# Performance work log

Hardware: AMD Instinct MI355X
Metric: run time of the kernel (lower is better)

The kernel has to match this reference:

```python
import jax, jax.numpy as jnp
import numpy as np
from jax.ops import segment_sum, segment_max

LRELU = 0.01  # torch F.leaky_relu default negative_slope


def _seg_softmax(e, seg, n):
    # torch_geometric.utils.softmax: stable segment softmax with 1e-16 eps
    m = segment_max(e, seg, num_segments=n)
    ex = jnp.exp(e - m[seg])
    s = segment_sum(ex, seg, num_segments=n)
    return ex / (s[seg] + 1e-16)


def _gcn(x, ei, w):
    j, i = ei[0], ei[1]  # code unpacks (edge_index_j, edge_index_i)
    n = x.shape[0]
    deg = segment_sum(jnp.ones_like(x[:, 0])[i], i, num_segments=n)
    dis = jnp.where(deg > 0, deg ** -0.5, 0.0)
    norm = dis[j] * dis[i]
    agg = segment_sum(norm[:, None] * x[j], i, num_segments=n)  # out[i] += norm*x[j]
    return jax.nn.relu(agg) @ w


def _highway(x1, x2, w, b):
    gate = jax.nn.sigmoid(x1 @ w + b)
    return gate * x2 + (1.0 - gate) * x1


def _gat_r(x, ei, a_i, a_j):
    j, i = ei[0], ei[1]
    n = x.shape[0]
    si = x @ a_i  # [R]
    sj = x @ a_j
    e = si[i] + sj[j]
    alpha = _seg_softmax(jax.nn.leaky_relu(e, LRELU).astype(jnp.float32), j, n)  # grouped by j!
    return jax.nn.relu(segment_sum(alpha[:, None] * x[j], i, num_segments=n))


def _graphattention_wjq(x, ei, rel_all, rel_emb, ww1):
    i, j = ei[0], ei[1]  # this module unpacks (i, j)
    n = x.shape[0]
    ef = jax.nn.leaky_relu(x, LRELU)
    re = jax.nn.leaky_relu(rel_emb, LRELU)
    feat = jnp.concatenate([ef[i], re[rel_all], ef[j]], axis=1)  # [E, 700]
    att = _seg_softmax(feat @ ww1, i, n)
    return segment_sum(feat * att[:, None], i, num_segments=n)  # [N, 700]


def _gat(x, r, ei, rel, a_i, a_j, a_r):
    j, i = ei[0], ei[1]
    n = x.shape[0]
    e = (x @ a_i)[i] + (x @ a_j)[j] + (r @ a_r)[rel]
    alpha = _seg_softmax(jax.nn.leaky_relu(e, LRELU).astype(jnp.float32), i, n)
    return jax.nn.relu(segment_sum(alpha[:, None] * x[j], i, num_segments=n))


def setup_inputs() -> dict:
    key = jax.random.key(0)
    ks = jax.random.split(key, 24)
    N, E, R, ELG, EH, RH = 20000, 150000, 1000, 15000, 300, 100

    def edges(k, n_nodes, n_edges):
        k1, k2 = jax.random.split(k)
        src = jax.random.randint(k1, (n_edges,), 0, n_nodes)
        dst = jax.random.randint(k2, (n_edges,), 0, n_nodes)
        src = jnp.where(src == dst, (src + 1) % n_nodes, src)  # no self-loops
        ring = jnp.arange(n_nodes)  # guarantee in-degree >= 1 everywhere
        src = src.at[:n_nodes].set((ring + 1) % n_nodes)
        dst = dst.at[:n_nodes].set(ring)
        return jnp.stack([src, dst])  # row0 = j (source), row1 = i (target)

    rel = jax.random.randint(ks[3], (E,), 0, R).at[0].set(R - 1)  # branch -> rel_emb1
    p = lambda k, sh: (jax.random.normal(k, sh, jnp.float32) * 0.05)
    return {
        "x_e": jax.random.normal(ks[0], (N, EH), jnp.float32),
        "edge_index": edges(ks[1], N, E),
        "rel": rel,
        "edge_index_all": edges(ks[2], N, E),
        "rel_all": jax.random.randint(ks[4], (E,), 0, 2 * R),
        "line_graph_index_out": edges(ks[5], R, ELG),
        "line_graph_val_out": jax.random.normal(ks[6], (ELG,), jnp.float32),
        "line_graph_index_in": edges(ks[7], R, ELG),
        "line_graph_val_in": jax.random.normal(ks[8], (ELG,), jnp.float32),
        "gcn1_w": p(ks[9], (EH, EH)),
        "gcn2_w": p(ks[10], (EH, EH)),
        "hw1_w": p(ks[11], (EH, EH)),
        "hw1_b": jnp.zeros((EH,), jnp.float32),
        "hw2_w": p(ks[12], (EH, EH)),
        "hw2_b": jnp.zeros((EH,), jnp.float32),
        "ww1": p(ks[13], (2 * EH + RH,)),
        "gat_ai": p(ks[14], (2 * (2 * EH + RH) - 400 + 0,)) if False else p(ks[14], (1000,)),
        "gat_aj": p(ks[15], (1000,)),
        "gat_ar": p(ks[16], (RH,)),
        "gatr_ai": p(ks[17], (RH,)),
        "gatr_aj": p(ks[18], (RH,)),
        "rel_emb1": p(ks[19], (R, RH)),
        "rel_emb2": p(ks[20], (R, RH)),
    }


def reference(x_e, edge_index, rel, edge_index_all, rel_all,
              line_graph_index_out, line_graph_val_out,
              line_graph_index_in, line_graph_val_in,
              gcn1_w, gcn2_w, hw1_w, hw1_b, hw2_w, hw2_b, ww1,
              gat_ai, gat_aj, gat_ar, gatr_ai, gatr_aj, rel_emb1, rel_emb2):
    # RAGA.forward; inputs constructed so rel.max()+1 == rel_emb1.shape[0]
    # (branch taken) and edge_index_all has no self-loops (remove_self_loops no-op).
    x = _highway(x_e, _gcn(x_e, edge_index_all, gcn1_w), hw1_w, hw1_b)
    x = _highway(x, _gcn(x, edge_index_all, gcn2_w), hw2_w, hw2_b)
    rel_emb_out = _gat_r(rel_emb1, line_graph_index_out, gatr_ai, gatr_aj)
    rel_emb_in = _gat_r(rel_emb1, line_graph_index_in, gatr_ai, gatr_aj)
    rel_emb = jnp.concatenate([rel_emb_out, rel_emb_in], axis=0)  # [2R, 100]
    x_wjq = jnp.concatenate(
        [x, _graphattention_wjq(x, edge_index_all, rel_all, rel_emb, ww1)], axis=1)  # [N, 1000]
    out = jnp.concatenate(
        [x_wjq, _gat(x_wjq, rel_emb, edge_index_all, rel_all, gat_ai, gat_aj, gat_ar)], axis=1)
    return out  # [N, 2000]
```

## Files before the change

kernel.cpp:

```cpp
#include <hip/hip_runtime.h>
#include <math.h>

#define LSL 0.01f

typedef _Float16 half8 __attribute__((ext_vector_type(8)));
typedef _Float16 half2 __attribute__((ext_vector_type(2)));
typedef float floatx4 __attribute__((ext_vector_type(4)));

static __device__ __forceinline__ float lrelu_f(float x){ return x > 0.f ? x : LSL * x; }
static __device__ __forceinline__ void atomAddF(float* p, float v){ unsafeAtomicAdd(p, v); }

static __device__ __forceinline__ unsigned encF(float f){
  unsigned u = __float_as_uint(f);
  return (u & 0x80000000u) ? ~u : (u | 0x80000000u);
}
static __device__ __forceinline__ float decF(unsigned u){
  return (u & 0x80000000u) ? __uint_as_float(u & 0x7FFFFFFFu) : __uint_as_float(~u);
}

__global__ void k_count2(const int* __restrict__ dstA, const int* __restrict__ srcA,
                         int* __restrict__ degD, int* __restrict__ degS, int E){
  int e = blockIdx.x * blockDim.x + threadIdx.x;
  if (e < E){ atomicAdd(degD + dstA[e], 1); atomicAdd(degS + srcA[e], 1); }
}

__global__ __launch_bounds__(1024)
void k_scan2(const int* __restrict__ cntD, int* __restrict__ offD,
             const int* __restrict__ cntS, int* __restrict__ offS, int n){
  const int* cnt = blockIdx.x ? cntS : cntD;
  int* off = blockIdx.x ? offS : offD;
  int t = threadIdx.x, lane = t & 63, wid = t >> 6;
  int len = (n + 1023) >> 10;
  int lo = t * len, hi = min(lo + len, n);
  int s = 0;
  for (int k = lo; k < hi; k++) s += cnt[k];
  int ws = s;
  #pragma unroll
  for (int o = 1; o < 64; o <<= 1){
    int u = __shfl_up(ws, o);
    if (lane >= o) ws += u;
  }
  __shared__ int wtot[16];
  if (lane == 63) wtot[wid] = ws;
  __syncthreads();
  int wpre = 0;
  #pragma unroll
  for (int k2 = 0; k2 < 16; k2++) wpre += (k2 < wid) ? wtot[k2] : 0;
  int run = wpre + ws - s;
  for (int k = lo; k < hi; k++){ off[k] = run; run += cnt[k]; }
  if (t == 0){
    int tot = 0;
    #pragma unroll
    for (int k2 = 0; k2 < 16; k2++) tot += wtot[k2];
    off[n] = tot;
  }
}

__global__ void k_fill2(const int* __restrict__ dstA, const int* __restrict__ srcA,
                        const int* __restrict__ offD, const int* __restrict__ offS,
                        int* __restrict__ curD, int* __restrict__ curS,
                        int* __restrict__ permD, int* __restrict__ permS, int E){
  int e = blockIdx.x * blockDim.x + threadIdx.x;
  if (e >= E) return;
  int i = dstA[e];
  permD[offD[i] + atomicAdd(curD + i, 1)] = e;
  int j = srcA[e];
  permS[offS[j] + atomicAdd(curS + j, 1)] = e;
}

__global__ void k_inv_sqrt_int(const int* __restrict__ deg, float* __restrict__ dis, int N){
  int v = blockIdx.x * blockDim.x + threadIdx.x;
  if (v < N){ int d = deg[v]; dis[v] = d > 0 ? rsqrtf((float)d) : 0.f; }
}

__global__ __launch_bounds__(256)
void k_conv_f16(const float* __restrict__ x, _Float16* __restrict__ xh, int N){
  int i = blockIdx.x, t = threadIdx.x;
  _Float16* o = xh + (size_t)i * 320;
  if (i < N){
    const float* r = x + (size_t)i * 300;
    o[t] = (_Float16)r[t];
    if (t < 44) o[t + 256] = (_Float16)r[t + 256];
    else if (t < 64) o[t + 256] = (_Float16)0.f;
  } else {
    o[t] = (_Float16)0.f;
    if (t < 64) o[t + 256] = (_Float16)0.f;
  }
}

__global__ __launch_bounds__(256)
void k_gcn_gather(const int* __restrict__ off, const int* __restrict__ perm,
                  const int* __restrict__ src, const _Float16* __restrict__ x,
                  const float* __restrict__ dis, _Float16* __restrict__ agg, int N){
  int i = (int)(((long)blockIdx.x * blockDim.x + threadIdx.x) >> 6);
  int lane = threadIdx.x & 63;
  if (i >= N) return;
  int p0 = off[i], p1 = off[i+1];
  float di = dis[i];
  float acc[8] = {0.f,0.f,0.f,0.f,0.f,0.f,0.f,0.f};
  for (int base = p0; base < p1; base += 64){
    int m = min(64, p1 - base);
    int jj = 0; float wl = 0.f;
    if (base + lane < p1){
      int e = perm[base + lane];
      jj = src[e];
      wl = di * dis[jj];
    }
    int q = 0;
    for (; q + 1 < m; q += 2){
      int j0 = __shfl(jj, q),   j1 = __shfl(jj, q+1);
      float w0 = __shfl(wl, q), w1 = __shfl(wl, q+1);
      if (lane < 40){
        half8 v0 = *(const half8*)(x + (size_t)j0 * 320 + 8*lane);
        half8 v1 = *(const half8*)(x + (size_t)j1 * 320 + 8*lane);
        #pragma unroll
        for (int k = 0; k < 8; k++) acc[k] += w0 * (float)v0[k] + w1 * (float)v1[k];
      }
    }
    if (q < m){
      int j0 = __shfl(jj, q);
      float w0 = __shfl(wl, q);
      if (lane < 40){
        half8 v0 = *(const half8*)(x + (size_t)j0 * 320 + 8*lane);
        #pragma unroll
        for (int k = 0; k < 8; k++) acc[k] += w0 * (float)v0[k];
      }
    }
  }
  if (lane < 40){
    half8 o;
    #pragma unroll
    for (int k = 0; k < 8; k++) o[k] = (_Float16)fmaxf(acc[k], 0.f);
    *(half8*)(agg + (size_t)i * 320 + 8*lane) = o;
  }
}

__global__ void k_prep_B4(const float* __restrict__ W0, const float* __restrict__ W1,
                          const float* __restrict__ W2, const float* __restrict__ W3,
                          _Float16* __restrict__ BfAll){
  int idx = blockIdx.x * 256 + threadIdx.x;
  if (idx >= 4*12800) return;
  int wsel = idx / 12800;
  int rem2 = idx % 12800;
  const float* W = (wsel == 0) ? W0 : (wsel == 1) ? W1 : (wsel == 2) ? W2 : W3;
  int lane = rem2 & 63;
  int rem = rem2 >> 6;
  int nf = rem & 3; rem >>= 2;
  int nt = rem % 5;
  int ks = rem / 5;
  int n = nt*64 + nf*16 + (lane & 15);
  int kb = ks*32 + (lane >> 4) * 8;
  _Float16* o = BfAll + (size_t)wsel * 102400 + (size_t)rem2 * 8;
  #pragma unroll
  for (int e = 0; e < 8; e++){
    int k = kb + e;
    float v = (k < 300 && n < 300) ? W[(size_t)k * 300 + n] : 0.f;
    o[e] = (_Float16)v;
  }
}

__global__ __launch_bounds__(256)
void k_dual_mfma(const _Float16* __restrict__ A1, const _Float16* __restrict__ Xh,
                 const _Float16* __restrict__ Bf1, const _Float16* __restrict__ Bf2,
                 const float* __restrict__ bias, float* __restrict__ Of32, long ldo,
                 _Float16* __restrict__ Oh, long ldm, int M){
  int nb = gridDim.x;
  int q = nb >> 3, r = nb & 7;
  int xcd = blockIdx.x & 7, kk0 = blockIdx.x >> 3;
  int pseudo = (xcd < r ? xcd * (q + 1) : r * (q + 1) + (xcd - r) * q) + kk0;
  int nt = pseudo % 5;
  int panel = pseudo / 5;

  int tid = threadIdx.x;
  int w = tid >> 6, lane = tid & 63;
  int l15 = lane & 15, lg = lane >> 4;
  int rowBase = panel * 64 + w * 16;
  int colBase = nt * 64;

  floatx4 acc1[4], acc2[4];
  #pragma unroll
  for (int b = 0; b < 4; b++){
    acc1[b] = (floatx4){0.f,0.f,0.f,0.f};
    acc2[b] = (floatx4){0.f,0.f,0.f,0.f};
  }

  int row0 = rowBase + l15;
  const _Float16* a1p0 = A1 + (size_t)row0 * 320;
  const _Float16* a2p0 = Xh + (size_t)row0 * 320;

  for (int ks = 0; ks < 10; ks++){
    int kA = ks*32 + lg*8;
    half8 a1f0 = *(const half8*)(a1p0 + kA);
    half8 a2f0 = *(const half8*)(a2p0 + kA);
    const half8* b1p = (const half8*)Bf1 + ((size_t)(ks*5 + nt) * 4 * 64 + lane);
    const half8* b2p = (const half8*)Bf2 + ((size_t)(ks*5 + nt) * 4 * 64 + lane);
    #pragma unroll
    for (int nf = 0; nf < 4; nf++){
      half8 b1 = b1p[nf*64];
      half8 b2 = b2p[nf*64];
      acc1[nf] = __builtin_amdgcn_mfma_f32_16x16x32_f16(a1f0, b1, acc1[nf], 0,0,0);
      acc2[nf] = __builtin_amdgcn_mfma_f32_16x16x32_f16(a2f0, b2, acc2[nf], 0,0,0);
    }
  }

  #pragma unroll
  for (int nf = 0; nf < 4; nf++){
    int gn = colBase + nf*16 + l15;
    int gnc = min(gn, 299);
    float bv = bias[gnc];
    #pragma unroll
    for (int r2 = 0; r2 < 4; r2++){
      int gm = rowBase + lg*4 + r2;
      int gmc = min(gm, M-1);
      float xv = (float)Xh[(size_t)gmc * 320 + gnc];
      float g = 1.f / (1.f + expf(-(acc2[nf][r2] + bv)));
      float val = g * acc1[nf][r2] + (1.f - g) * xv;
      if (gm < M && gn < 300){
        if (Of32) Of32[(size_t)gm * ldo + gn] = val;
        if (Oh)   Oh[(size_t)gm * ldm + gn] = (_Float16)val;
      }
    }
  }
}

__global__ __launch_bounds__(256)
void k_wjq_gather(const int* __restrict__ off, const int* __restrict__ perm,
                  const int* __restrict__ dstA, const int* __restrict__ relI,
                  const float* __restrict__ sxi, const float* __restrict__ sxj,
                  const float* __restrict__ aRel, const float* __restrict__ relEmb,
                  const float* __restrict__ gat_ai, const float* __restrict__ gat_aj,
                  float* __restrict__ out, _Float16* __restrict__ xh2,
                  float* __restrict__ gxi, float* __restrict__ gxj, int N){
  int i = (int)(((long)blockIdx.x * blockDim.x + threadIdx.x) >> 6);
  int lane = threadIdx.x & 63;
  if (i >= N) return;
  int p0 = off[i], p1 = off[i+1];
  int deg = p1 - p0;
  float si = sxi[i];
  float accx[8] = {0.f,0.f,0.f,0.f,0.f,0.f,0.f,0.f};
  float accr[4] = {0.f,0.f,0.f,0.f};
  float sumA;

  if (deg <= 64){
    int jj = 0, rr = 0; float l = -3.4e38f;
    if (lane < deg){
      int e = perm[p0 + lane];
      jj = dstA[e]; rr = relI[e];
      l = si + sxj[jj] + aRel[rr];
    }
    float lm = l;
    #pragma unroll
    for (int o = 32; o > 0; o >>= 1) lm = fmaxf(lm, __shfl_xor(lm, o));
    float exl = (lane < deg) ? expf(l - lm) : 0.f;
    float ls = exl;
    #pragma unroll
    for (int o = 32; o > 0; o >>= 1) ls += __shfl_xor(ls, o);
    float inv = 1.f / (ls + 1e-16f);
    sumA = ls * inv;
    float wgt = exl * inv;
    int qe = 0;
    for (; qe + 1 < deg; qe += 2){
      int j0 = __shfl(jj, qe),  j1 = __shfl(jj, qe+1);
      int r0 = __shfl(rr, qe),  r1 = __shfl(rr, qe+1);
      float a0 = __shfl(wgt, qe), a1 = __shfl(wgt, qe+1);
      if (lane < 38){
        half8 v0 = *(const half8*)(xh2 + (size_t)j0 * 1024 + 8*lane);
        half8 v1 = *(const half8*)(xh2 + (size_t)j1 * 1024 + 8*lane);
        #pragma unroll
        for (int k = 0; k < 8; k++)
          accx[k] += a0 * lrelu_f((float)v0[k]) + a1 * lrelu_f((float)v1[k]);
      } else if (lane < 63){
        floatx4 v0 = *(const floatx4*)(relEmb + (size_t)r0 * 100 + 4*(lane - 38));
        floatx4 v1 = *(const floatx4*)(relEmb + (size_t)r1 * 100 + 4*(lane - 38));
        #pragma unroll
        for (int k = 0; k < 4; k++)
          accr[k] += a0 * lrelu_f(v0[k]) + a1 * lrelu_f(v1[k]);
      }
    }
    if (qe < deg){
      int j0 = __shfl(jj, qe);
      int r0 = __shfl(rr, qe);
      float a0 = __shfl(wgt, qe);
      if (lane < 38){
        half8 v0 = *(const half8*)(xh2 + (size_t)j0 * 1024 + 8*lane);
        #pragma unroll
        for (int k = 0; k < 8; k++) accx[k] += a0 * lrelu_f((float)v0[k]);
      } else if (lane < 63){
        floatx4 v0 = *(const floatx4*)(relEmb + (size_t)r0 * 100 + 4*(lane - 38));
        #pragma unroll
        for (int k = 0; k < 4; k++) accr[k] += a0 * lrelu_f(v0[k]);
      }
    }
  } else {
    float lm = -3.4e38f;
    for (int p = p0 + lane; p < p1; p += 64){
      int e = perm[p];
      lm = fmaxf(lm, si + sxj[dstA[e]] + aRel[relI[e]]);
    }
    #pragma unroll
    for (int o = 32; o > 0; o >>= 1) lm = fmaxf(lm, __shfl_xor(lm, o));
    float ls = 0.f;
    for (int p = p0 + lane; p < p1; p += 64){
      int e = perm[p];
      ls += expf(si + sxj[dstA[e]] + aRel[relI[e]] - lm);
    }
    #pragma unroll
    for (int o = 32; o > 0; o >>= 1) ls += __shfl_xor(ls, o);
    float inv = 1.f / (ls + 1e-16f);
    sumA = ls * inv;
    for (int base = p0; base < p1; base += 64){
      int m = min(64, p1 - base);
      int jj = 0, rr = 0; float all = 0.f;
      if (base + lane < p1){
        int e = perm[base + lane];
        jj = dstA[e]; rr = relI[e];
        all = expf(si + sxj[jj] + aRel[rr] - lm) * inv;
      }
      for (int qe = 0; qe < m; qe++){
        int j = __shfl(jj, qe);
        int r = __shfl(rr, qe);
        float al = __shfl(all, qe);
        if (lane < 38){
          half8 v = *(const half8*)(xh2 + (size_t)j * 1024 + 8*lane);
          #pragma unroll
          for (int k = 0; k < 8; k++) accx[k] += al * lrelu_f((float)v[k]);
        } else if (lane < 63){
          floatx4 v = *(const floatx4*)(relEmb + (size_t)r * 100 + 4*(lane - 38));
          #pragma unroll
          for (int k = 0; k < 4; k++) accr[k] += al * lrelu_f(v[k]);
        }
      }
    }
  }

  float* oi = out + (size_t)i * 2000;
  _Float16* hi = xh2 + (size_t)i * 1024;
  float dA = 0.f, dB = 0.f;
  if (lane < 38){
    #pragma unroll
    for (int k = 0; k < 8; k++){
      int c = 8*lane + k;
      if (c < 300){
        oi[700 + c] = accx[k]; hi[700 + c] = (_Float16)accx[k];
        dA += accx[k] * gat_ai[700 + c];
        dB += accx[k] * gat_aj[700 + c];
      }
    }
    half8 v = *(const half8*)(hi + 8*lane);
    #pragma unroll
    for (int k = 0; k < 8; k++){
      int c = 8*lane + k;
      if (c < 300){
        float x2v = (float)v[k];
        float h = lrelu_f(x2v) * sumA;
        oi[300 + c] = h; hi[300 + c] = (_Float16)h;
        dA += x2v * gat_ai[c] + h * gat_ai[300 + c];
        dB += x2v * gat_aj[c] + h * gat_aj[300 + c];
      }
    }
  } else if (lane < 63){
    #pragma unroll
    for (int k = 0; k < 4; k++){
      int c = 4*(lane - 38) + k;
      oi[600 + c] = accr[k]; hi[600 + c] = (_Float16)accr[k];
      dA += accr[k] * gat_ai[600 + c];
      dB += accr[k] * gat_aj[600 + c];
    }
  }
  #pragma unroll
  for (int o = 32; o > 0; o >>= 1){
    dA += __shfl_xor(dA, o);
    dB += __shfl_xor(dB, o);
  }
  if (lane == 0){ gxi[i] = dA; gxj[i] = dB; }
}

__global__ __launch_bounds__(256)
void k_gat_gather(const int* __restrict__ off, const int* __restrict__ perm,
                  const int* __restrict__ srcA, const int* __restrict__ relI,
                  const float* __restrict__ gxi, const float* __restrict__ gxj,
                  const float* __restrict__ srr, const _Float16* __restrict__ xh2,
                  float* __restrict__ out, int N){
  long gw = ((long)blockIdx.x * blockDim.x + threadIdx.x) >> 6;
  int lane = threadIdx.x & 63;
  int i = (int)(gw >> 1), half = (int)(gw & 1);
  if (i >= N) return;
  int p0 = off[i], p1 = off[i+1];
  int deg = p1 - p0;
  float gi = gxi[i];
  int colBase = half * 512;
  int c0 = colBase + 8*lane;
  bool act = c0 < 1000;
  float acc[8] = {0.f,0.f,0.f,0.f,0.f,0.f,0.f,0.f};

  if (deg <= 64){
    int jj = 0; float l = -3.4e38f;
    if (lane < deg){
      int e = perm[p0 + lane];
      jj = srcA[e];
      l = lrelu_f(gi + gxj[jj] + srr[relI[e]]);
    }
    float lm = l;
    #pragma unroll
    for (int o = 32; o > 0; o >>= 1) lm = fmaxf(lm, __shfl_xor(lm, o));
    float exl = (lane < deg) ? expf(l - lm) : 0.f;
    float ls = exl;
    #pragma unroll
    for (int o = 32; o > 0; o >>= 1) ls += __shfl_xor(ls, o);
    float wgt = exl / (ls + 1e-16f);
    int qe = 0;
    for (; qe + 1 < deg; qe += 2){
      int j0 = __shfl(jj, qe),    j1 = __shfl(jj, qe+1);
      float a0 = __shfl(wgt, qe), a1 = __shfl(wgt, qe+1);
      if (act){
        half8 v0 = *(const half8*)(xh2 + (size_t)j0 * 1024 + c0);
        half8 v1 = *(const half8*)(xh2 + (size_t)j1 * 1024 + c0);
        #pragma unroll
        for (int k = 0; k < 8; k++) acc[k] += a0 * (float)v0[k] + a1 * (float)v1[k];
      }
    }
    if (qe < deg){
      int j0 = __shfl(jj, qe);
      float a0 = __shfl(wgt, qe);
      if (act){
        half8 v0 = *(const half8*)(xh2 + (size_t)j0 * 1024 + c0);
        #pragma unroll
        for (int k = 0; k < 8; k++) acc[k] += a0 * (float)v0[k];
      }
    }
  } else {
    float lm = -3.4e38f;
    for (int p = p0 + lane; p < p1; p += 64){
      int e = perm[p];
      lm = fmaxf(lm, lrelu_f(gi + gxj[srcA[e]] + srr[relI[e]]));
    }
    #pragma unroll
    for (int o = 32; o > 0; o >>= 1) lm = fmaxf(lm, __shfl_xor(lm, o));
    float ls = 0.f;
    for (int p = p0 + lane; p < p1; p += 64){
      int e = perm[p];
      ls += expf(lrelu_f(gi + gxj[srcA[e]] + srr[relI[e]]) - lm);
    }
    #pragma unroll
    for (int o = 32; o > 0; o >>= 1) ls += __shfl_xor(ls, o);
    float inv = 1.f / (ls + 1e-16f);
    for (int base = p0; base < p1; base += 64){
      int m = min(64, p1 - base);
      int jj = 0; float all = 0.f;
      if (base + lane < p1){
        int e = perm[base + lane];
        jj = srcA[e];
        all = expf(lrelu_f(gi + gxj[jj] + srr[relI[e]]) - lm) * inv;
      }
      for (int qe = 0; qe < m; qe++){
        int j = __shfl(jj, qe);
        float al = __shfl(all, qe);
        if (act){
          half8 v = *(const half8*)(xh2 + (size_t)j * 1024 + c0);
          #pragma unroll
          for (int k = 0; k < 8; k++) acc[k] += al * (float)v[k];
        }
      }
    }
  }

  if (act){
    float* oi = out + (size_t)i * 2000 + 1000 + c0;
    floatx4 s0, s1;
    #pragma unroll
    for (int k = 0; k < 4; k++){ s0[k] = fmaxf(acc[k], 0.f); s1[k] = fmaxf(acc[4+k], 0.f); }
    *(floatx4*)(oi) = s0;
    *(floatx4*)(oi + 4) = s1;
  }
}

__global__ void k_dot2_small(const float* __restrict__ X, int ld, int len,
                             const float* __restrict__ wA, const float* __restrict__ wB,
                             float* __restrict__ oA, float* __restrict__ oB,
                             int n, int applyL){
  int v = blockIdx.x * blockDim.x + threadIdx.x;
  if (v >= n) return;
  const float* row = X + (size_t)v * ld;
  float a = 0.f, b = 0.f;
  for (int c = 0; c < len; c++){
    float f = row[c];
    if (applyL) f = lrelu_f(f);
    a += f * wA[c];
    if (wB) b += f * wB[c];
  }
  oA[v] = a;
  if (oB) oB[v] = b;
}

__global__ void k_relu_dots(float* __restrict__ relEmb, const float* __restrict__ wA,
                            const float* __restrict__ wB, float* __restrict__ aRel,
                            float* __restrict__ srr, int n){
  int v = blockIdx.x * blockDim.x + threadIdx.x;
  if (v >= n) return;
  float* row = relEmb + (size_t)v * 100;
  float a = 0.f, b = 0.f;
  for (int c = 0; c < 100; c++){
    float f = fmaxf(row[c], 0.f);
    row[c] = f;
    a += f * wA[c];
    b += f * wB[c];
  }
  aRel[v] = a;
  srr[v] = b;
}

__global__ void k_wave_dot2_h(const _Float16* __restrict__ X, long ld, int len,
                              const float* __restrict__ wA, const float* __restrict__ wB,
                              float* __restrict__ oA, float* __restrict__ oB,
                              int n, int applyL){
  int gw = (int)(((long)blockIdx.x * blockDim.x + threadIdx.x) >> 6);
  int lane = threadIdx.x & 63;
  if (gw >= n) return;
  const _Float16* row = X + (size_t)gw * ld;
  float a = 0.f, b = 0.f;
  for (int c = lane*2; c < len; c += 128){
    half2 v = *(const half2*)(row + c);
    float f0 = (float)v[0], f1 = (float)v[1];
    if (applyL){ f0 = lrelu_f(f0); f1 = lrelu_f(f1); }
    a += f0 * wA[c] + f1 * wA[c+1];
    b += f0 * wB[c] + f1 * wB[c+1];
  }
  #pragma unroll
  for (int o = 32; o > 0; o >>= 1){
    a += __shfl_down(a, o);
    b += __shfl_down(b, o);
  }
  if (lane == 0){ oA[gw] = a; oB[gw] = b; }
}

__global__ void k_lg_logit(const int* __restrict__ lgOut, const int* __restrict__ lgIn,
                           int ELG, int R, const float* __restrict__ sR_i,
                           const float* __restrict__ sR_j,
                           float* __restrict__ elog, unsigned* __restrict__ mEnc){
  int e = blockIdx.x * blockDim.x + threadIdx.x;
  if (e >= 2*ELG) return;
  int g = e >= ELG;
  int el = e - g*ELG;
  const int* lg = g ? lgIn : lgOut;
  int j = lg[el], i = lg[el + ELG];
  float v = lrelu_f(sR_j[j] + sR_i[i]);
  elog[e] = v;
  atomicMax(mEnc + g*R + j, encF(v));
}

__global__ void k_lg_exp(const int* __restrict__ lgOut, const int* __restrict__ lgIn,
                         int ELG, int R, float* __restrict__ elog,
                         const unsigned* __restrict__ mEnc, float* __restrict__ sumR){
  int e = blockIdx.x * blockDim.x + threadIdx.x;
  if (e >= 2*ELG) return;
  int g = e >= ELG;
  int el = e - g*ELG;
  const int* lg = g ? lgIn : lgOut;
  int j = lg[el];
  float ex = expf(elog[e] - decF(mEnc[g*R + j]));
  elog[e] = ex;
  atomAddF(sumR + g*R + j, ex);
}

__global__ void k_lg_scatter(const int* __restrict__ lgOut, const int* __restrict__ lgIn,
                             int ELG, int R, const float* __restrict__ ex,
                             const float* __restrict__ sumR,
                             const float* __restrict__ relEmb1, float* __restrict__ relEmb){
  int e = blockIdx.x;
  int g = e >= ELG;
  int el = e - g*ELG;
  const int* lg = g ? lgIn : lgOut;
  int j = lg[el], i = lg[el + ELG];
  float alpha = ex[e] / (sumR[g*R + j] + 1e-16f);
  const float* xj = relEmb1 + (size_t)j * 100;
  float* oi = relEmb + (size_t)(g*R + i) * 100;
  for (int c = threadIdx.x; c < 100; c += blockDim.x)
    atomAddF(oi + c, alpha * xj[c]);
}

extern "C" void kernel_launch(void* const* d_in, const int* in_sizes, int n_in,
                              void* d_out, int out_size, void* d_ws, size_t ws_size,
                              hipStream_t stream){
  const float* x_e     = (const float*)d_in[0];
  const int*   eiA     = (const int*)  d_in[3];
  const int*   relAll  = (const int*)  d_in[4];
  const int*   lgOut   = (const int*)  d_in[5];
  const int*   lgIn    = (const int*)  d_in[7];
  const float* gcn1_w  = (const float*)d_in[9];
  const float* gcn2_w  = (const float*)d_in[10];
  const float* hw1_w   = (const float*)d_in[11];
  const float* hw1_b   = (const float*)d_in[12];
  const float* hw2_w   = (const float*)d_in[13];
  const float* hw2_b   = (const float*)d_in[14];
  const float* ww1     = (const float*)d_in[15];
  const float* gat_ai  = (const float*)d_in[16];
  const float* gat_aj  = (const float*)d_in[17];
  const float* gat_ar  = (const float*)d_in[18];
  const float* gatr_ai = (const float*)d_in[19];
  const float* gatr_aj = (const float*)d_in[20];
  const float* relEmb1 = (const float*)d_in[21];

  const int EH = 300, RH = 100;
  const int N   = in_sizes[0] / EH;
  const int E   = in_sizes[3] / 2;
  const int ELG = in_sizes[5] / 2;
  const int R   = in_sizes[21] / RH;
  const int Mtiles = (N + 127) / 128;
  const int Mpad = Mtiles * 128;

  char* base = (char*)d_ws;
  _Float16* xh0   = (_Float16*)base;  base += (size_t)Mpad * 320 * 2;
  _Float16* xhA   = (_Float16*)base;  base += (size_t)Mpad * 320 * 2;
  _Float16* A1f16 = (_Float16*)base;  base += (size_t)Mpad * 320 * 2;
  _Float16* xh2   = (_Float16*)base;  base += (size_t)N * 1024 * 2;
  _Float16* BfAll = (_Float16*)base;  base += (size_t)4 * 102400 * 2;
  float* w = (float*)base;
  float* dis    = w; w += N;
  float* relEmb = w; w += (size_t)2 * R * RH;
  float* sxi    = w; w += N;
  float* sxj    = w; w += N;
  float* gxi    = w; w += N;
  float* gxj    = w; w += N;
  float* sR_i   = w; w += R;
  float* sR_j   = w; w += R;
  unsigned* mEncR = (unsigned*)w; w += 2 * R;
  float* sumR   = w; w += 2 * R;
  float* aRel   = w; w += 2 * R;
  float* srr    = w; w += 2 * R;
  float* eE     = w; w += E;
  int* degD   = (int*)w; w += N;
  int* degS   = (int*)w; w += N;
  int* curD   = (int*)w; w += N;
  int* curS   = (int*)w; w += N;
  int* offD   = (int*)w; w += N + 1;
  int* offS   = (int*)w; w += N + 1;
  int* permD  = (int*)w; w += E;
  int* permS  = (int*)w; w += E;

  _Float16* Bf_g1 = BfAll;
  _Float16* Bf_h1 = BfAll + 102400;
  _Float16* Bf_g2 = BfAll + 2 * 102400;
  _Float16* Bf_h2 = BfAll + 3 * 102400;

  float* out = (float*)d_out;
  const int* srcA = eiA;
  const int* dstA = eiA + E;

  auto cdiv = [](int a, int b){ return (a + b - 1) / b; };

  hipMemsetAsync(degD, 0, (size_t)4 * N * 4, stream);
  k_count2<<<cdiv(E,256),256,0,stream>>>(dstA, srcA, degD, degS, E);
  k_scan2<<<2,1024,0,stream>>>(degD, offD, degS, offS, N);
  k_fill2<<<cdiv(E,256),256,0,stream>>>(dstA, srcA, offD, offS, curD, curS, permD, permS, E);
  k_inv_sqrt_int<<<cdiv(N,256),256,0,stream>>>(degD, dis, N);

  k_prep_B4<<<200,256,0,stream>>>(gcn1_w, hw1_w, gcn2_w, hw2_w, BfAll);
  k_conv_f16<<<Mpad,256,0,stream>>>(x_e, xh0, N);

  int NB = 5 * (Mpad / 64);
  int GW = cdiv(N, 4);

  k_gcn_gather<<<GW,256,0,stream>>>(offD, permD, srcA, xh0, dis, A1f16, N);
  k_dual_mfma<<<NB,256,0,stream>>>(A1f16, xh0, Bf_g1, Bf_h1, hw1_b,
                                   nullptr, 0, xhA, 320, N);

  k_gcn_gather<<<GW,256,0,stream>>>(offD, permD, srcA, xhA, dis, A1f16, N);
  k_dual_mfma<<<NB,256,0,stream>>>(A1f16, xhA, Bf_g2, Bf_h2, hw2_b,
                                   out, 2000, xh2, 1024, N);

  k_dot2_small<<<cdiv(R,256),256,0,stream>>>(relEmb1, RH, RH, gatr_ai, gatr_aj, sR_i, sR_j, R, 0);
  hipMemsetAsync(relEmb, 0, (size_t)2*R*RH*4, stream);
  hipMemsetAsync(mEncR, 0, (size_t)4*R*4, stream);
  k_lg_logit<<<cdiv(2*ELG,256),256,0,stream>>>(lgOut, lgIn, ELG, R, sR_i, sR_j, eE, mEncR);
  k_lg_exp<<<cdiv(2*ELG,256),256,0,stream>>>(lgOut, lgIn, ELG, R, eE, mEncR, sumR);
  k_lg_scatter<<<2*ELG,128,0,stream>>>(lgOut, lgIn, ELG, R, eE, sumR, relEmb1, relEmb);

  k_relu_dots<<<cdiv(2*R,256),256,0,stream>>>(relEmb, ww1 + EH, gat_ar, aRel, srr, 2*R);

  k_wave_dot2_h<<<cdiv(N,4),256,0,stream>>>(xh2, 1024, EH, ww1, ww1 + EH + RH, sxi, sxj, N, 1);

  k_wjq_gather<<<GW,256,0,stream>>>(offS, permS, dstA, relAll, sxi, sxj, aRel, relEmb,
                                    gat_ai, gat_aj, out, xh2, gxi, gxj, N);

  k_gat_gather<<<cdiv(N,2),256,0,stream>>>(offD, permD, srcA, relAll, gxi, gxj, srr, xh2, out, N);
}
```

Baseline: 404.1 us.

## Fuse small kernels, drop softmax max pass, recompute wjq features in GAT gather

```diff
diff --git a/kernel.cpp b/kernel.cpp
--- a/kernel.cpp
+++ b/kernel.cpp
@@ -4,19 +4,11 @@
 #define LSL 0.01f
 
 typedef _Float16 half8 __attribute__((ext_vector_type(8)));
-typedef _Float16 half2 __attribute__((ext_vector_type(2)));
+typedef _Float16 half4 __attribute__((ext_vector_type(4)));
 typedef float floatx4 __attribute__((ext_vector_type(4)));
 
 static __device__ __forceinline__ float lrelu_f(float x){ return x > 0.f ? x : LSL * x; }
 static __device__ __forceinline__ void atomAddF(float* p, float v){ unsafeAtomicAdd(p, v); }
-
-static __device__ __forceinline__ unsigned encF(float f){
-  unsigned u = __float_as_uint(f);
-  return (u & 0x80000000u) ? ~u : (u | 0x80000000u);
-}
-static __device__ __forceinline__ float decF(unsigned u){
-  return (u & 0x80000000u) ? __uint_as_float(u & 0x7FFFFFFFu) : __uint_as_float(~u);
-}
 
 __global__ void k_count2(const int* __restrict__ dstA, const int* __restrict__ srcA,
                          int* __restrict__ degD, int* __restrict__ degS, int E){
@@ -56,25 +48,29 @@
   }
 }
 
-__global__ void k_fill2(const int* __restrict__ dstA, const int* __restrict__ srcA,
-                        const int* __restrict__ offD, const int* __restrict__ offS,
-                        int* __restrict__ curD, int* __restrict__ curS,
-                        int* __restrict__ permD, int* __restrict__ permS, int E){
-  int e = blockIdx.x * blockDim.x + threadIdx.x;
-  if (e >= E) return;
-  int i = dstA[e];
-  permD[offD[i] + atomicAdd(curD + i, 1)] = e;
-  int j = srcA[e];
-  permS[offS[j] + atomicAdd(curS + j, 1)] = e;
-}
-
-__global__ void k_inv_sqrt_int(const int* __restrict__ deg, float* __restrict__ dis, int N){
-  int v = blockIdx.x * blockDim.x + threadIdx.x;
-  if (v < N){ int d = deg[v]; dis[v] = d > 0 ? rsqrtf((float)d) : 0.f; }
+__global__ void k_fill_inv(const int* __restrict__ dstA, const int* __restrict__ srcA,
+                           const int* __restrict__ offD, const int* __restrict__ offS,
+                           int* __restrict__ curD, int* __restrict__ curS,
+                           int* __restrict__ permD, int* __restrict__ permS,
+                           const int* __restrict__ degD, float* __restrict__ dis,
+                           int E, int N, int FB){
+  int b = blockIdx.x, t = threadIdx.x;
+  if (b < FB){
+    int e = b * 256 + t;
+    if (e >= E) return;
+    int i = dstA[e];
+    permD[offD[i] + atomicAdd(curD + i, 1)] = e;
+    int j = srcA[e];
+    permS[offS[j] + atomicAdd(curS + j, 1)] = e;
+  } else {
+    int v = (b - FB) * 256 + t;
+    if (v < N){ int d = degD[v]; dis[v] = d > 0 ? rsqrtf((float)d) : 0.f; }
+  }
 }
 
 __global__ __launch_bounds__(256)
-void k_conv_f16(const float* __restrict__ x, _Float16* __restrict__ xh, int N){
+void k_conv_f16(const float* __restrict__ x, _Float16* __restrict__ xh,
+                float* __restrict__ sxi, float* __restrict__ sxj, int N){
   int i = blockIdx.x, t = threadIdx.x;
   _Float16* o = xh + (size_t)i * 320;
   if (i < N){
@@ -82,6 +78,8 @@
     o[t] = (_Float16)r[t];
     if (t < 44) o[t + 256] = (_Float16)r[t + 256];
     else if (t < 64) o[t + 256] = (_Float16)0.f;
+    if (t == 0) sxi[i] = 0.f;
+    if (t == 1) sxj[i] = 0.f;
   } else {
     o[t] = (_Float16)0.f;
     if (t < 64) o[t + 256] = (_Float16)0.f;
@@ -163,7 +161,9 @@
 void k_dual_mfma(const _Float16* __restrict__ A1, const _Float16* __restrict__ Xh,
                  const _Float16* __restrict__ Bf1, const _Float16* __restrict__ Bf2,
                  const float* __restrict__ bias, float* __restrict__ Of32, long ldo,
-                 _Float16* __restrict__ Oh, long ldm, int M){
+                 _Float16* __restrict__ Oh, long ldm, int M,
+                 const float* __restrict__ ww, float* __restrict__ sxi,
+                 float* __restrict__ sxj){
   int nb = gridDim.x;
   int q = nb >> 3, r = nb & 7;
   int xcd = blockIdx.x & 7, kk0 = blockIdx.x >> 3;
@@ -203,11 +203,15 @@
     }
   }
 
+  bool doSX = (sxi != nullptr);
+  float dA[4] = {0.f,0.f,0.f,0.f}, dB[4] = {0.f,0.f,0.f,0.f};
   #pragma unroll
   for (int nf = 0; nf < 4; nf++){
     int gn = colBase + nf*16 + l15;
     int gnc = min(gn, 299);
     float bv = bias[gnc];
+    float wA = doSX ? ww[gnc] : 0.f;
+    float wB = doSX ? ww[400 + gnc] : 0.f;
     #pragma unroll
     for (int r2 = 0; r2 < 4; r2++){
       int gm = rowBase + lg*4 + r2;
@@ -218,6 +222,25 @@
       if (gm < M && gn < 300){
         if (Of32) Of32[(size_t)gm * ldo + gn] = val;
         if (Oh)   Oh[(size_t)gm * ldm + gn] = (_Float16)val;
+        float f = lrelu_f(val);
+        dA[r2] += f * wA;
+        dB[r2] += f * wB;
+      }
+    }
+  }
+  if (doSX){
+    #pragma unroll
+    for (int r2 = 0; r2 < 4; r2++){
+      float a = dA[r2], b = dB[r2];
+      #pragma unroll
+      for (int o = 1; o < 16; o <<= 1){
+        a += __shfl_xor(a, o);
+        b += __shfl_xor(b, o);
+      }
+      int gm = rowBase + lg*4 + r2;
+      if (l15 == 0 && gm < M){
+        atomAddF(sxi + gm, a);
+        atomAddF(sxj + gm, b);
       }
     }
   }
@@ -227,10 +250,11 @@
 void k_wjq_gather(const int* __restrict__ off, const int* __restrict__ perm,
                   const int* __restrict__ dstA, const int* __restrict__ relI,
                   const float* __restrict__ sxi, const float* __restrict__ sxj,
-                  const float* __restrict__ aRel, const float* __restrict__ relEmb,
+                  const float* __restrict__ aRel, const _Float16* __restrict__ relEmbH,
                   const float* __restrict__ gat_ai, const float* __restrict__ gat_aj,
                   float* __restrict__ out, _Float16* __restrict__ xh2,
-                  float* __restrict__ gxi, float* __restrict__ gxj, int N){
+                  float* __restrict__ gxi, float* __restrict__ gxj,
+                  float* __restrict__ sAl, int N){
   int i = (int)(((long)blockIdx.x * blockDim.x + threadIdx.x) >> 6);
   int lane = threadIdx.x & 63;
   if (i >= N) return;
@@ -270,11 +294,11 @@
         for (int k = 0; k < 8; k++)
           accx[k] += a0 * lrelu_f((float)v0[k]) + a1 * lrelu_f((float)v1[k]);
       } else if (lane < 63){
-        floatx4 v0 = *(const floatx4*)(relEmb + (size_t)r0 * 100 + 4*(lane - 38));
-        floatx4 v1 = *(const floatx4*)(relEmb + (size_t)r1 * 100 + 4*(lane - 38));
+        half4 v0 = *(const half4*)(relEmbH + (size_t)r0 * 100 + 4*(lane - 38));
+        half4 v1 = *(const half4*)(relEmbH + (size_t)r1 * 100 + 4*(lane - 38));
         #pragma unroll
         for (int k = 0; k < 4; k++)
-          accr[k] += a0 * lrelu_f(v0[k]) + a1 * lrelu_f(v1[k]);
+          accr[k] += a0 * (float)v0[k] + a1 * (float)v1[k];
       }
     }
     if (qe < deg){
@@ -286,9 +310,9 @@
         #pragma unroll
         for (int k = 0; k < 8; k++) accx[k] += a0 * lrelu_f((float)v0[k]);
       } else if (lane < 63){
-        floatx4 v0 = *(const floatx4*)(relEmb + (size_t)r0 * 100 + 4*(lane - 38));
+        half4 v0 = *(const half4*)(relEmbH + (size_t)r0 * 100 + 4*(lane - 38));
         #pragma unroll
-        for (int k = 0; k < 4; k++) accr[k] += a0 * lrelu_f(v0[k]);
+        for (int k = 0; k < 4; k++) accr[k] += a0 * (float)v0[k];
       }
     }
   } else {
@@ -325,9 +349,9 @@
           #pragma unroll
           for (int k = 0; k < 8; k++) accx[k] += al * lrelu_f((float)v[k]);
         } else if (lane < 63){
-          floatx4 v = *(const floatx4*)(relEmb + (size_t)r * 100 + 4*(lane - 38));
+          half4 v = *(const half4*)(relEmbH + (size_t)r * 100 + 4*(lane - 38));
           #pragma unroll
-          for (int k = 0; k < 4; k++) accr[k] += al * lrelu_f(v[k]);
+          for (int k = 0; k < 4; k++) accr[k] += al * (float)v[k];
         }
       }
     }
@@ -353,7 +377,7 @@
       if (c < 300){
         float x2v = (float)v[k];
         float h = lrelu_f(x2v) * sumA;
-        oi[300 + c] = h; hi[300 + c] = (_Float16)h;
+        oi[300 + c] = h;
         dA += x2v * gat_ai[c] + h * gat_ai[300 + c];
         dB += x2v * gat_aj[c] + h * gat_aj[300 + c];
       }
@@ -372,15 +396,15 @@
     dA += __shfl_xor(dA, o);
     dB += __shfl_xor(dB, o);
   }
-  if (lane == 0){ gxi[i] = dA; gxj[i] = dB; }
+  if (lane == 0){ gxi[i] = dA; gxj[i] = dB; sAl[i] = sumA; }
 }
 
 __global__ __launch_bounds__(256)
 void k_gat_gather(const int* __restrict__ off, const int* __restrict__ perm,
                   const int* __restrict__ srcA, const int* __restrict__ relI,
                   const float* __restrict__ gxi, const float* __restrict__ gxj,
-                  const float* __restrict__ srr, const _Float16* __restrict__ xh2,
-                  float* __restrict__ out, int N){
+                  const float* __restrict__ srr, const float* __restrict__ sAl,
+                  const _Float16* __restrict__ xh2, float* __restrict__ out, int N){
   long gw = ((long)blockIdx.x * blockDim.x + threadIdx.x) >> 6;
   int lane = threadIdx.x & 63;
   int i = (int)(gw >> 1), half = (int)(gw & 1);
@@ -388,17 +412,16 @@
   int p0 = off[i], p1 = off[i+1];
   int deg = p1 - p0;
   float gi = gxi[i];
-  int colBase = half * 512;
-  int c0 = colBase + 8*lane;
-  bool act = c0 < 1000;
-  float acc[8] = {0.f,0.f,0.f,0.f,0.f,0.f,0.f,0.f};
+  float acc_a[8] = {0.f,0.f,0.f,0.f,0.f,0.f,0.f,0.f};
+  float acc_b[8] = {0.f,0.f,0.f,0.f,0.f,0.f,0.f,0.f};
 
   if (deg <= 64){
-    int jj = 0; float l = -3.4e38f;
+    int jj = 0; float l = -3.4e38f, saj = 0.f;
     if (lane < deg){
       int e = perm[p0 + lane];
       jj = srcA[e];
       l = lrelu_f(gi + gxj[jj] + srr[relI[e]]);
+      if (half == 0) saj = sAl[jj];
     }
     float lm = l;
     #pragma unroll
@@ -408,24 +431,57 @@
     #pragma unroll
     for (int o = 32; o > 0; o >>= 1) ls += __shfl_xor(ls, o);
     float wgt = exl / (ls + 1e-16f);
-    int qe = 0;
-    for (; qe + 1 < deg; qe += 2){
-      int j0 = __shfl(jj, qe),    j1 = __shfl(jj, qe+1);
-      float a0 = __shfl(wgt, qe), a1 = __shfl(wgt, qe+1);
-      if (act){
-        half8 v0 = *(const half8*)(xh2 + (size_t)j0 * 1024 + c0);
-        half8 v1 = *(const half8*)(xh2 + (size_t)j1 * 1024 + c0);
-        #pragma unroll
-        for (int k = 0; k < 8; k++) acc[k] += a0 * (float)v0[k] + a1 * (float)v1[k];
-      }
-    }
-    if (qe < deg){
-      int j0 = __shfl(jj, qe);
-      float a0 = __shfl(wgt, qe);
-      if (act){
-        half8 v0 = *(const half8*)(xh2 + (size_t)j0 * 1024 + c0);
-        #pragma unroll
-        for (int k = 0; k < 8; k++) acc[k] += a0 * (float)v0[k];
+    if (half == 0){
+      int qe = 0;
+      for (; qe + 1 < deg; qe += 2){
+        int j0 = __shfl(jj, qe),    j1 = __shfl(jj, qe+1);
+        float a0 = __shfl(wgt, qe), a1 = __shfl(wgt, qe+1);
+        float s0 = __shfl(saj, qe) * a0, s1 = __shfl(saj, qe+1) * a1;
+        if (lane < 38){
+          half8 v0 = *(const half8*)(xh2 + (size_t)j0 * 1024 + 8*lane);
+          half8 v1 = *(const half8*)(xh2 + (size_t)j1 * 1024 + 8*lane);
+          #pragma unroll
+          for (int k = 0; k < 8; k++){
+            float x0 = (float)v0[k], x1 = (float)v1[k];
+            acc_a[k] += a0 * x0 + a1 * x1;
+            acc_b[k] += s0 * lrelu_f(x0) + s1 * lrelu_f(x1);
+          }
+        }
+      }
+      if (qe < deg){
+        int j0 = __shfl(jj, qe);
+        float a0 = __shfl(wgt, qe);
+        float s0 = __shfl(saj, qe) * a0;
+        if (lane < 38){
+          half8 v0 = *(const half8*)(xh2 + (size_t)j0 * 1024 + 8*lane);
+          #pragma unroll
+          for (int k = 0; k < 8; k++){
+            float x0 = (float)v0[k];
+            acc_a[k] += a0 * x0;
+            acc_b[k] += s0 * lrelu_f(x0);
+          }
+        }
+      }
+    } else {
+      int qe = 0;
+      for (; qe + 1 < deg; qe += 2){
+        int j0 = __shfl(jj, qe),    j1 = __shfl(jj, qe+1);
+        float a0 = __shfl(wgt, qe), a1 = __shfl(wgt, qe+1);
+        if (lane < 50){
+          half8 v0 = *(const half8*)(xh2 + (size_t)j0 * 1024 + 600 + 8*lane);
+          half8 v1 = *(const half8*)(xh2 + (size_t)j1 * 1024 + 600 + 8*lane);
+          #pragma unroll
+          for (int k = 0; k < 8; k++) acc_a[k] += a0 * (float)v0[k] + a1 * (float)v1[k];
+        }
+      }
+      if (qe < deg){
+        int j0 = __shfl(jj, qe);
+        float a0 = __shfl(wgt, qe);
+        if (lane < 50){
+          half8 v0 = *(const half8*)(xh2 + (size_t)j0 * 1024 + 600 + 8*lane);
+          #pragma unroll
+          for (int k = 0; k < 8; k++) acc_a[k] += a0 * (float)v0[k];
+        }
       }
     }
   } else {
@@ -446,31 +502,66 @@
     float inv = 1.f / (ls + 1e-16f);
     for (int base = p0; base < p1; base += 64){
       int m = min(64, p1 - base);
-      int jj = 0; float all = 0.f;
+      int jj = 0; float all = 0.f, saj = 0.f;
       if (base + lane < p1){
         int e = perm[base + lane];
         jj = srcA[e];
         all = expf(lrelu_f(gi + gxj[jj] + srr[relI[e]]) - lm) * inv;
+        if (half == 0) saj = sAl[jj];
       }
       for (int qe = 0; qe < m; qe++){
         int j = __shfl(jj, qe);
         float al = __shfl(all, qe);
-        if (act){
-          half8 v = *(const half8*)(xh2 + (size_t)j * 1024 + c0);
-          #pragma unroll
-          for (int k = 0; k < 8; k++) acc[k] += al * (float)v[k];
+        if (half == 0){
+          float sa = __shfl(saj, qe) * al;
+          if (lane < 38){
+            half8 v = *(const half8*)(xh2 + (size_t)j * 1024 + 8*lane);
+            #pragma unroll
+            for (int k = 0; k < 8; k++){
+              float x0 = (float)v[k];
+              acc_a[k] += al * x0;
+              acc_b[k] += sa * lrelu_f(x0);
+            }
+          }
+        } else {
+          if (lane < 50){
+            half8 v = *(const half8*)(xh2 + (size_t)j * 1024 + 600 + 8*lane);
+            #pragma unroll
+            for (int k = 0; k < 8; k++) acc_a[k] += al * (float)v[k];
+          }
         }
       }
     }
   }
 
-  if (act){
-    float* oi = out + (size_t)i * 2000 + 1000 + c0;
-    floatx4 s0, s1;
-    #pragma unroll
-    for (int k = 0; k < 4; k++){ s0[k] = fmaxf(acc[k], 0.f); s1[k] = fmaxf(acc[4+k], 0.f); }
-    *(floatx4*)(oi) = s0;
-    *(floatx4*)(oi + 4) = s1;
+  float* ob = out + (size_t)i * 2000 + 1000;
+  if (half == 0){
+    if (lane < 37){
+      floatx4 s0, s1, t0, t1;
+      #pragma unroll
+      for (int k = 0; k < 4; k++){
+        s0[k] = fmaxf(acc_a[k], 0.f);   s1[k] = fmaxf(acc_a[4+k], 0.f);
+        t0[k] = fmaxf(acc_b[k], 0.f);   t1[k] = fmaxf(acc_b[4+k], 0.f);
+      }
+      *(floatx4*)(ob + 8*lane) = s0;
+      *(floatx4*)(ob + 8*lane + 4) = s1;
+      *(floatx4*)(ob + 300 + 8*lane) = t0;
+      *(floatx4*)(ob + 300 + 8*lane + 4) = t1;
+    } else if (lane == 37){
+      #pragma unroll
+      for (int k = 0; k < 4; k++){
+        ob[296 + k] = fmaxf(acc_a[k], 0.f);
+        ob[596 + k] = fmaxf(acc_b[k], 0.f);
+      }
+    }
+  } else {
+    if (lane < 50){
+      floatx4 s0, s1;
+      #pragma unroll
+      for (int k = 0; k < 4; k++){ s0[k] = fmaxf(acc_a[k], 0.f); s1[k] = fmaxf(acc_a[4+k], 0.f); }
+      *(floatx4*)(ob + 600 + 8*lane) = s0;
+      *(floatx4*)(ob + 600 + 8*lane + 4) = s1;
+    }
   }
 }
 
@@ -492,16 +583,18 @@
   if (oB) oB[v] = b;
 }
 
-__global__ void k_relu_dots(float* __restrict__ relEmb, const float* __restrict__ wA,
-                            const float* __restrict__ wB, float* __restrict__ aRel,
-                            float* __restrict__ srr, int n){
+__global__ void k_relu_dots(float* __restrict__ relEmb, _Float16* __restrict__ relEmbH,
+                            const float* __restrict__ wA, const float* __restrict__ wB,
+                            float* __restrict__ aRel, float* __restrict__ srr, int n){
   int v = blockIdx.x * blockDim.x + threadIdx.x;
   if (v >= n) return;
   float* row = relEmb + (size_t)v * 100;
+  _Float16* rowH = relEmbH + (size_t)v * 100;
   float a = 0.f, b = 0.f;
   for (int c = 0; c < 100; c++){
     float f = fmaxf(row[c], 0.f);
     row[c] = f;
+    rowH[c] = (_Float16)f;
     a += f * wA[c];
     b += f * wB[c];
   }
@@ -509,55 +602,17 @@
   srr[v] = b;
 }
 
-__global__ void k_wave_dot2_h(const _Float16* __restrict__ X, long ld, int len,
-                              const float* __restrict__ wA, const float* __restrict__ wB,
-                              float* __restrict__ oA, float* __restrict__ oB,
-                              int n, int applyL){
-  int gw = (int)(((long)blockIdx.x * blockDim.x + threadIdx.x) >> 6);
-  int lane = threadIdx.x & 63;
-  if (gw >= n) return;
-  const _Float16* row = X + (size_t)gw * ld;
-  float a = 0.f, b = 0.f;
-  for (int c = lane*2; c < len; c += 128){
-    half2 v = *(const half2*)(row + c);
-    float f0 = (float)v[0], f1 = (float)v[1];
-    if (applyL){ f0 = lrelu_f(f0); f1 = lrelu_f(f1); }
-    a += f0 * wA[c] + f1 * wA[c+1];
-    b += f0 * wB[c] + f1 * wB[c+1];
-  }
-  #pragma unroll
-  for (int o = 32; o > 0; o >>= 1){
-    a += __shfl_down(a, o);
-    b += __shfl_down(b, o);
-  }
-  if (lane == 0){ oA[gw] = a; oB[gw] = b; }
-}
-
-__global__ void k_lg_logit(const int* __restrict__ lgOut, const int* __restrict__ lgIn,
-                           int ELG, int R, const float* __restrict__ sR_i,
-                           const float* __restrict__ sR_j,
-                           float* __restrict__ elog, unsigned* __restrict__ mEnc){
+__global__ void k_lg_le(const int* __restrict__ lgOut, const int* __restrict__ lgIn,
+                        int ELG, int R, const float* __restrict__ sR_i,
+                        const float* __restrict__ sR_j,
+                        float* __restrict__ elog, float* __restrict__ sumR){
   int e = blockIdx.x * blockDim.x + threadIdx.x;
   if (e >= 2*ELG) return;
   int g = e >= ELG;
   int el = e - g*ELG;
   const int* lg = g ? lgIn : lgOut;
   int j = lg[el], i = lg[el + ELG];
-  float v = lrelu_f(sR_j[j] + sR_i[i]);
-  elog[e] = v;
-  atomicMax(mEnc + g*R + j, encF(v));
-}
-
-__global__ void k_lg_exp(const int* __restrict__ lgOut, const int* __restrict__ lgIn,
-                         int ELG, int R, float* __restrict__ elog,
-                         const unsigned* __restrict__ mEnc, float* __restrict__ sumR){
-  int e = blockIdx.x * blockDim.x + threadIdx.x;
-  if (e >= 2*ELG) return;
-  int g = e >= ELG;
-  int el = e - g*ELG;
-  const int* lg = g ? lgIn : lgOut;
-  int j = lg[el];
-  float ex = expf(elog[e] - decF(mEnc[g*R + j]));
+  float ex = expf(lrelu_f(sR_j[j] + sR_i[i]));
   elog[e] = ex;
   atomAddF(sumR + g*R + j, ex);
 }
@@ -614,17 +669,18 @@
   _Float16* A1f16 = (_Float16*)base;  base += (size_t)Mpad * 320 * 2;
   _Float16* xh2   = (_Float16*)base;  base += (size_t)N * 1024 * 2;
   _Float16* BfAll = (_Float16*)base;  base += (size_t)4 * 102400 * 2;
+  _Float16* relEmbH = (_Float16*)base; base += (size_t)2 * R * RH * 2;
   float* w = (float*)base;
   float* dis    = w; w += N;
   float* relEmb = w; w += (size_t)2 * R * RH;
+  float* sumR   = w; w += 2 * R;
   float* sxi    = w; w += N;
   float* sxj    = w; w += N;
   float* gxi    = w; w += N;
   float* gxj    = w; w += N;
+  float* sAl    = w; w += N;
   float* sR_i   = w; w += R;
   float* sR_j   = w; w += R;
-  unsigned* mEncR = (unsigned*)w; w += 2 * R;
-  float* sumR   = w; w += 2 * R;
   float* aRel   = w; w += 2 * R;
   float* srr    = w; w += 2 * R;
   float* eE     = w; w += E;
@@ -651,36 +707,34 @@
   hipMemsetAsync(degD, 0, (size_t)4 * N * 4, stream);
   k_count2<<<cdiv(E,256),256,0,stream>>>(dstA, srcA, degD, degS, E);
   k_scan2<<<2,1024,0,stream>>>(degD, offD, degS, offS, N);
-  k_fill2<<<cdiv(E,256),256,0,stream>>>(dstA, srcA, offD, offS, curD, curS, permD, permS, E);
-  k_inv_sqrt_int<<<cdiv(N,256),256,0,stream>>>(degD, dis, N);
+  int FB = cdiv(E,256);
+  k_fill_inv<<<FB + cdiv(N,256),256,0,stream>>>(dstA, srcA, offD, offS, curD, curS,
+                                                permD, permS, degD, dis, E, N, FB);
 
   k_prep_B4<<<200,256,0,stream>>>(gcn1_w, hw1_w, gcn2_w, hw2_w, BfAll);
-  k_conv_f16<<<Mpad,256,0,stream>>>(x_e, xh0, N);
+  k_conv_f16<<<Mpad,256,0,stream>>>(x_e, xh0, sxi, sxj, N);
 
   int NB = 5 * (Mpad / 64);
   int GW = cdiv(N, 4);
 
   k_gcn_gather<<<GW,256,0,stream>>>(offD, permD, srcA, xh0, dis, A1f16, N);
   k_dual_mfma<<<NB,256,0,stream>>>(A1f16, xh0, Bf_g1, Bf_h1, hw1_b,
-                                   nullptr, 0, xhA, 320, N);
+                                   nullptr, 0, xhA, 320, N, nullptr, nullptr, nullptr);
 
   k_gcn_gather<<<GW,256,0,stream>>>(offD, permD, srcA, xhA, dis, A1f16, N);
   k_dual_mfma<<<NB,256,0,stream>>>(A1f16, xhA, Bf_g2, Bf_h2, hw2_b,
-                                   out, 2000, xh2, 1024, N);
+                                   out, 2000, xh2, 1024, N, ww1, sxi, sxj);
 
   k_dot2_small<<<cdiv(R,256),256,0,stream>>>(relEmb1, RH, RH, gatr_ai, gatr_aj, sR_i, sR_j, R, 0);
-  hipMemsetAsync(relEmb, 0, (size_t)2*R*RH*4, stream);
-  hipMemsetAsync(mEncR, 0, (size_t)4*R*4, stream);
-  k_lg_logit<<<cdiv(2*ELG,256),256,0,stream>>>(lgOut, lgIn, ELG, R, sR_i, sR_j, eE, mEncR);
-  k_lg_exp<<<cdiv(2*ELG,256),256,0,stream>>>(lgOut, lgIn, ELG, R, eE, mEncR, sumR);
+  hipMemsetAsync(relEmb, 0, ((size_t)2*R*RH + 2*R) * 4, stream);
+  k_lg_le<<<cdiv(2*ELG,256),256,0,stream>>>(lgOut, lgIn, ELG, R, sR_i, sR_j, eE, sumR);
   k_lg_scatter<<<2*ELG,128,0,stream>>>(lgOut, lgIn, ELG, R, eE, sumR, relEmb1, relEmb);
 
-  k_relu_dots<<<cdiv(2*R,256),256,0,stream>>>(relEmb, ww1 + EH, gat_ar, aRel, srr, 2*R);
-
-  k_wave_dot2_h<<<cdiv(N,4),256,0,stream>>>(xh2, 1024, EH, ww1, ww1 + EH + RH, sxi, sxj, N, 1);
-
-  k_wjq_gather<<<GW,256,0,stream>>>(offS, permS, dstA, relAll, sxi, sxj, aRel, relEmb,
-                                    gat_ai, gat_aj, out, xh2, gxi, gxj, N);
-
-  k_gat_gather<<<cdiv(N,2),256,0,stream>>>(offD, permD, srcA, relAll, gxi, gxj, srr, xh2, out, N);
-}
+  k_relu_dots<<<cdiv(2*R,256),256,0,stream>>>(relEmb, relEmbH, ww1 + EH, gat_ar, aRel, srr, 2*R);
+
+  k_wjq_gather<<<GW,256,0,stream>>>(offS, permS, dstA, relAll, sxi, sxj, aRel, relEmbH,
+                                    gat_ai, gat_aj, out, xh2, gxi, gxj, sAl, N);
+
+  k_gat_gather<<<cdiv(N,2),256,0,stream>>>(offD, permD, srcA, relAll, gxi, gxj, srr,
+                                           sAl, xh2, out, N);
+}
```

New measurement: 392.4 us. 1.03x faster.
